# Optimization experiments

Measured on AMD Instinct MI355X. Metric: run time of the kernel, lower is better.

## Reference

```python
import jax, jax.numpy as jnp
import numpy as np

B, D_IN = 16384, 1024
N_DOM, EMB = 4, 16
H1, H2, H3 = 512, 256, 128
FH = 64
EPS = 1e-5


def setup_inputs() -> dict:
    key = jax.random.key(0)
    ks = jax.random.split(key, 32)
    s = 0.02
    def rn(k, shape):
        return jax.random.normal(k, shape, dtype=jnp.float32) * s
    inp = {
        "x": jax.random.normal(ks[0], (B, D_IN), dtype=jnp.float32),
        "domain_ids": jax.random.randint(ks[1], (B,), 0, N_DOM),
        # PartitionedNormalization params
        "pn_w": jnp.ones((N_DOM, D_IN), jnp.float32),
        "pn_b": jnp.zeros((N_DOM, D_IN), jnp.float32),
        # center net: D_IN->512->256->128
        "cW1": rn(ks[2], (D_IN, H1)), "cb1": jnp.zeros((H1,), jnp.float32),
        "cW2": rn(ks[3], (H1, H2)),  "cb2": jnp.zeros((H2,), jnp.float32),
        "cW3": rn(ks[4], (H2, H3)),  "cb3": jnp.zeros((H3,), jnp.float32),
        # domain-specific nets, stacked over domains
        "dW1": rn(ks[5], (N_DOM, D_IN, H1)), "db1": jnp.zeros((N_DOM, H1), jnp.float32),
        "dW2": rn(ks[6], (N_DOM, H1, H2)),  "db2": jnp.zeros((N_DOM, H2), jnp.float32),
        "dW3": rn(ks[7], (N_DOM, H2, H3)),  "db3": jnp.full((N_DOM, H3), 1.0, jnp.float32),  # domain_net_init_bias=1.0
        # final mlp: 128->64->1
        "fW1": rn(ks[8], (H3, FH)), "fb1": jnp.zeros((FH,), jnp.float32),
        "fW2": rn(ks[9], (FH, 1)),  "fb2": jnp.zeros((1,), jnp.float32),
        # domain embedding + auxiliary net: 16->32->1
        "dom_emb": rn(ks[10], (N_DOM, EMB)),
        "aW1": rn(ks[11], (EMB, 32)), "ab1": jnp.zeros((32,), jnp.float32),
        "aW2": rn(ks[12], (32, 1)),   "ab2": jnp.zeros((1,), jnp.float32),
    }
    return inp


def _forward(x, domain_ids, pn_w, pn_b,
             cW1, cb1, cW2, cb2, cW3, cb3,
             dW1, db1, dW2, db2, dW3, db3,
             fW1, fb1, fW2, fb2,
             dom_emb, aW1, ab1, aW2, ab2):
    # Partitioned normalization: per-sample layernorm over features,
    # domain-conditional affine (vectorized gather instead of python loop)
    mean = jnp.mean(x, axis=1, keepdims=True)
    var = jnp.mean(jnp.square(x - mean), axis=1, keepdims=True)  # unbiased=False
    norm = (x - mean) / jnp.sqrt(var + EPS)
    norm = norm * pn_w[domain_ids] + pn_b[domain_ids]  # (B, D_IN)

    # center net
    h = jax.nn.relu(norm @ cW1 + cb1)
    h = jax.nn.relu(h @ cW2 + cb2)
    h_center = h @ cW3 + cb3  # (B, H3)

    # domain-specific nets: compute all domains, then gather per-sample
    hd = jax.nn.relu(jnp.einsum('bi,dio->bdo', norm, dW1) + db1[None])   # (B,D,H1)
    hd = jax.nn.relu(jnp.einsum('bdi,dio->bdo', hd, dW2) + db2[None])    # (B,D,H2)
    hd = jnp.einsum('bdi,dio->bdo', hd, dW3) + db3[None]                 # (B,D,H3)
    h_domain = jnp.take_along_axis(hd, domain_ids[:, None, None], axis=1)[:, 0]  # (B,H3)

    h_fused = h_center * jnp.tanh(h_domain)

    main = jax.nn.relu(h_fused @ fW1 + fb1) @ fW2 + fb2  # (B,1)

    de = dom_emb[domain_ids]                              # (B,EMB)
    aux = jax.nn.relu(de @ aW1 + ab1) @ aW2 + ab2         # (B,1)

    return jax.nn.sigmoid(main + aux)


def reference(x, domain_ids, pn_w, pn_b,
              cW1, cb1, cW2, cb2, cW3, cb3,
              dW1, db1, dW2, db2, dW3, db3,
              fW1, fb1, fW2, fb2,
              dom_emb, aW1, ab1, aW2, ab2):
    return _forward(x, domain_ids, pn_w, pn_b,
                    cW1, cb1, cW2, cb2, cW3, cb3,
                    dW1, db1, dW2, db2, dW3, db3,
                    fW1, fb1, fW2, fb2,
                    dom_emb, aW1, ab1, aW2, ab2)
```

## Files before the change

kernel.cpp:

```cpp
#include <hip/hip_runtime.h>
#include <hip/hip_bf16.h>
#include <stdint.h>

#define NB   16384
#define DIN  1024
#define MPAD 16896

typedef __bf16 bf16;
typedef __bf16 v8bf __attribute__((ext_vector_type(8)));
typedef float  v4f  __attribute__((ext_vector_type(4)));
typedef unsigned char u8;

typedef __attribute__((address_space(1))) void* as1_ptr;
typedef __attribute__((address_space(3))) void* as3_ptr;

__device__ __forceinline__ void gl_lds16(const void* g, void* l) {
  __builtin_amdgcn_global_load_lds((as1_ptr)(g), (as3_ptr)(l), 16, 0, 0);
}

__device__ __forceinline__ unsigned short bfbits(float f) {
  bf16 h = (bf16)f;
  return __builtin_bit_cast(unsigned short, h);
}

__device__ __forceinline__ unsigned short pk8(float a, float b) {
  int u = __builtin_amdgcn_cvt_pk_fp8_f32(a, b, 0, false);
  return (unsigned short)(u & 0xffff);
}

__global__ __launch_bounds__(1024) void k_sort(
    const int* __restrict__ dom, int* __restrict__ pstart_g,
    int* __restrict__ perm, int* __restrict__ rowpos, float* __restrict__ aux,
    const float* __restrict__ dom_emb, const float* __restrict__ aW1,
    const float* __restrict__ ab1, const float* __restrict__ aW2,
    const float* __restrict__ ab2) {
  __shared__ int sc0[1024], sc1[1024], sc2[1024], sc3[1024];
  const int tid = threadIdx.x;
  int dv[16];
  int c0 = 0, c1 = 0, c2 = 0, c3 = 0;
#pragma unroll
  for (int it = 0; it < 16; it++) {
    int d = dom[it * 1024 + tid];
    dv[it] = d;
    c0 += (d == 0); c1 += (d == 1); c2 += (d == 2); c3 += (d == 3);
  }
  sc0[tid] = c0; sc1[tid] = c1; sc2[tid] = c2; sc3[tid] = c3;
  for (int j = tid; j < MPAD; j += 1024) perm[j] = -1;
  __syncthreads();
  for (int off = 1; off < 1024; off <<= 1) {
    int v0 = (tid >= off) ? sc0[tid - off] : 0;
    int v1 = (tid >= off) ? sc1[tid - off] : 0;
    int v2 = (tid >= off) ? sc2[tid - off] : 0;
    int v3 = (tid >= off) ? sc3[tid - off] : 0;
    __syncthreads();
    sc0[tid] += v0; sc1[tid] += v1; sc2[tid] += v2; sc3[tid] += v3;
    __syncthreads();
  }
  const int t0 = sc0[1023], t1 = sc1[1023], t2 = sc2[1023];
  const int s1 = (t0 + 127) & ~127;
  const int s2 = s1 + ((t1 + 127) & ~127);
  const int s3 = s2 + ((t2 + 127) & ~127);
  int b0 = 0 + sc0[tid] - c0;
  int b1 = s1 + sc1[tid] - c1;
  int b2 = s2 + sc2[tid] - c2;
  int b3 = s3 + sc3[tid] - c3;
#pragma unroll
  for (int it = 0; it < 16; it++) {
    int i = it * 1024 + tid;
    int d = dv[it];
    int pos = (d == 0) ? b0++ : ((d == 1) ? b1++ : ((d == 2) ? b2++ : b3++));
    perm[pos] = i;
    rowpos[i] = pos;
  }
  if (tid == 0) {
    int t3 = sc3[1023];
    pstart_g[0] = 0; pstart_g[1] = s1; pstart_g[2] = s2; pstart_g[3] = s3;
    pstart_g[4] = s3 + ((t3 + 127) & ~127);
  }
  if (tid < 4) {
    float a = ab2[0];
    for (int j = 0; j < 32; j++) {
      float s = ab1[j];
      for (int i = 0; i < 16; i++) s += dom_emb[tid * 16 + i] * aW1[i * 32 + j];
      a += fmaxf(s, 0.f) * aW2[j];
    }
    aux[tid] = a;
  }
}

__global__ __launch_bounds__(256) void k_ln(const float* __restrict__ x,
                                            const int* __restrict__ dom,
                                            const int* __restrict__ rowpos,
                                            const float* __restrict__ pn_w,
                                            const float* __restrict__ pn_b,
                                            u8* __restrict__ norm) {
  int wv = threadIdx.x >> 6, lane = threadIdx.x & 63;
  int r = blockIdx.x * 4 + wv;
  const float* xr = x + (size_t)r * DIN;
  float4 v[4];
#pragma unroll
  for (int g = 0; g < 4; g++) v[g] = *(const float4*)(xr + g * 256 + lane * 4);
  float s = 0.f;
#pragma unroll
  for (int g = 0; g < 4; g++) s += v[g].x + v[g].y + v[g].z + v[g].w;
#pragma unroll
  for (int o = 32; o; o >>= 1) s += __shfl_xor(s, o, 64);
  float mean = s * (1.f / 1024.f);
  float q = 0.f;
#pragma unroll
  for (int g = 0; g < 4; g++) {
    float a = v[g].x - mean, b = v[g].y - mean, c = v[g].z - mean, e = v[g].w - mean;
    q += a * a + b * b + c * c + e * e;
  }
#pragma unroll
  for (int o = 32; o; o >>= 1) q += __shfl_xor(q, o, 64);
  float rstd = rsqrtf(q * (1.f / 1024.f) + 1e-5f);
  int d = dom[r];
  int pos = rowpos[r];
  const float* pw = pn_w + (size_t)d * DIN;
  const float* pb = pn_b + (size_t)d * DIN;
  u8* orow = norm + (size_t)pos * DIN;
#pragma unroll
  for (int g = 0; g < 4; g++) {
    float4 w4 = *(const float4*)(pw + g * 256 + lane * 4);
    float4 b4 = *(const float4*)(pb + g * 256 + lane * 4);
    float f0 = (v[g].x - mean) * rstd * w4.x + b4.x;
    float f1 = (v[g].y - mean) * rstd * w4.y + b4.y;
    float f2 = (v[g].z - mean) * rstd * w4.z + b4.z;
    float f3 = (v[g].w - mean) * rstd * w4.w + b4.w;
    int u = __builtin_amdgcn_cvt_pk_fp8_f32(f0, f1, 0, false);
    u = __builtin_amdgcn_cvt_pk_fp8_f32(f2, f3, u, true);
    *(unsigned int*)(orow + g * 256 + lane * 4) = (unsigned int)u;
  }
}

__global__ __launch_bounds__(256) void k_wt_all(
    const float* __restrict__ cW1, const float* __restrict__ cW2,
    const float* __restrict__ cW3, const float* __restrict__ dW1,
    const float* __restrict__ dW2, const float* __restrict__ dW3,
    const float* __restrict__ fW1,
    u8* __restrict__ cW1t, u8* __restrict__ cW2t, u8* __restrict__ cW3t,
    u8* __restrict__ dW1t, u8* __restrict__ dW2t, u8* __restrict__ dW3t,
    bf16* __restrict__ fW1t) {
  __shared__ float t[64 * 65];
  int bid = blockIdx.x;
  const float* src; u8* dst; int K, N, tile; bool isf = false;
  if (bid < 640) {
    K = 1024; N = 512; int m = bid >> 7; tile = bid & 127;
    src = m == 0 ? cW1 : dW1 + (size_t)(m - 1) * 524288;
    dst = m == 0 ? cW1t : dW1t + (size_t)(m - 1) * 524288;
  } else if (bid < 800) {
    K = 512; N = 256; int m = (bid - 640) >> 5; tile = (bid - 640) & 31;
    src = m == 0 ? cW2 : dW2 + (size_t)(m - 1) * 131072;
    dst = m == 0 ? cW2t : dW2t + (size_t)(m - 1) * 131072;
  } else if (bid < 840) {
    K = 256; N = 128; int m = (bid - 800) >> 3; tile = (bid - 800) & 7;
    src = m == 0 ? cW3 : dW3 + (size_t)(m - 1) * 32768;
    dst = m == 0 ? cW3t : dW3t + (size_t)(m - 1) * 32768;
  } else {
    K = 128; N = 64; tile = bid - 840; src = fW1; dst = nullptr; isf = true;
  }
  int ntn = N >> 6;
  int k0 = (tile / ntn) << 6, n0 = (tile % ntn) << 6;
  int tid = threadIdx.x;
  int r = tid >> 2, c4 = (tid & 3) << 4;
#pragma unroll
  for (int j4 = 0; j4 < 4; j4++) {
    float4 v = *(const float4*)(src + (size_t)(k0 + r) * N + n0 + c4 + j4 * 4);
    t[r * 65 + c4 + j4 * 4 + 0] = v.x;
    t[r * 65 + c4 + j4 * 4 + 1] = v.y;
    t[r * 65 + c4 + j4 * 4 + 2] = v.z;
    t[r * 65 + c4 + j4 * 4 + 3] = v.w;
  }
  __syncthreads();
  int n = tid >> 2, kc = (tid & 3) << 4;
  if (!isf) {
#pragma unroll
    for (int j4 = 0; j4 < 4; j4++) {
      float v0 = t[(kc + j4 * 4 + 0) * 65 + n] * 16.f;
      float v1 = t[(kc + j4 * 4 + 1) * 65 + n] * 16.f;
      float v2 = t[(kc + j4 * 4 + 2) * 65 + n] * 16.f;
      float v3 = t[(kc + j4 * 4 + 3) * 65 + n] * 16.f;
      int u = __builtin_amdgcn_cvt_pk_fp8_f32(v0, v1, 0, false);
      u = __builtin_amdgcn_cvt_pk_fp8_f32(v2, v3, u, true);
      *(unsigned int*)(dst + (size_t)(n0 + n) * K + k0 + kc + j4 * 4) = (unsigned int)u;
    }
  } else {
#pragma unroll
    for (int j4 = 0; j4 < 4; j4++) {
      ushort4 o;
      o.x = bfbits(t[(kc + j4 * 4 + 0) * 65 + n]);
      o.y = bfbits(t[(kc + j4 * 4 + 1) * 65 + n]);
      o.z = bfbits(t[(kc + j4 * 4 + 2) * 65 + n]);
      o.w = bfbits(t[(kc + j4 * 4 + 3) * 65 + n]);
      *(ushort4*)(fW1t + (size_t)(n0 + n) * K + k0 + kc + j4 * 4) = o;
    }
  }
}

__global__ __launch_bounds__(256) void k_gemm(const u8* __restrict__ A, int lda,
                                              int aoffc, int aoffd,
                                              const u8* __restrict__ cWt,
                                              const u8* __restrict__ dWt,
                                              const float* __restrict__ cb,
                                              const float* __restrict__ db,
                                              u8* __restrict__ C, int Nh, int Kd,
                                              int relu, const int* __restrict__ pstart,
                                              int lognct) {
  __shared__ __align__(16) u8 Al[128 * 64];
  __shared__ __align__(16) u8 Bl[128 * 64];
  const int tid = threadIdx.x;
  const int wv = tid >> 6, lane = tid & 63;
  const int nct = 1 << lognct;
  const int T1 = nct << 7;
  int l = blockIdx.x, rt, ct;
  if (l < T1) {
    int t = l >> 3;
    ct = t & (nct - 1);
    rt = ((t >> lognct) << 3) | (l & 7);
  } else {
    int l2 = l - T1;
    rt = 128 + (l2 >> lognct);
    ct = l2 & (nct - 1);
  }
  const int row0 = rt * 128;
  int d = 0;
  if (row0 >= pstart[1]) d = 1;
  if (row0 >= pstart[2]) d = 2;
  if (row0 >= pstart[3]) d = 3;
  const int n0 = ct * 128;
  const bool isd = (n0 >= Nh);
  const u8* Wt = isd ? dWt + ((size_t)d * Nh + (n0 - Nh)) * Kd : cWt + (size_t)n0 * Kd;
  const float* bias = isd ? db + d * Nh + (n0 - Nh) : cb + n0;
  const int aoff = isd ? aoffd : aoffc;
  const u8* Ab = A + (size_t)row0 * lda + aoff;

  v4f acc[4][4];
#pragma unroll
  for (int i = 0; i < 4; i++)
#pragma unroll
    for (int j = 0; j < 4; j++) acc[i][j] = v4f{0.f, 0.f, 0.f, 0.f};

  const int wm = (wv >> 1) * 64, wn = (wv & 1) * 64;
  const int mrow = lane & 15, quad = lane >> 4;
  const int lrow = lane >> 2;
  const int lchk = lane & 3;
  const int ldc = 2 * Nh;

  for (int kt = 0; kt < Kd; kt += 64) {
#pragma unroll
    for (int p = 0; p < 2; p++) {
      int rbase = wv * 32 + p * 16;
      int r = rbase + lrow;
      int jg = lchk ^ (r & 3);
      gl_lds16(Ab + (size_t)r * lda + kt + jg * 16, &Al[rbase * 64]);
      gl_lds16(Wt + (size_t)r * Kd + kt + jg * 16, &Bl[rbase * 64]);
    }
    __syncthreads();
#pragma unroll
    for (int s = 0; s < 2; s++) {
      long af[4], bfr[4];
#pragma unroll
      for (int mi = 0; mi < 4; mi++) {
        int m = wm + mi * 16 + mrow;
        int jc = s * 2 + (quad >> 1);
        int js = jc ^ (m & 3);
        af[mi] = *(const long*)&Al[m * 64 + js * 16 + (quad & 1) * 8];
      }
#pragma unroll
      for (int ni = 0; ni < 4; ni++) {
        int n = wn + ni * 16 + mrow;
        int jc = s * 2 + (quad >> 1);
        int js = jc ^ (n & 3);
        bfr[ni] = *(const long*)&Bl[n * 64 + js * 16 + (quad & 1) * 8];
      }
#pragma unroll
      for (int mi = 0; mi < 4; mi++)
#pragma unroll
        for (int ni = 0; ni < 4; ni++)
          acc[mi][ni] =
              __builtin_amdgcn_mfma_f32_16x16x32_fp8_fp8(af[mi], bfr[ni], acc[mi][ni], 0, 0, 0);
    }
    __syncthreads();
  }

  float bv[4];
#pragma unroll
  for (int ni = 0; ni < 4; ni++) bv[ni] = bias[wn + ni * 16 + mrow];
#pragma unroll
  for (int mi = 0; mi < 4; mi++) {
    int growb = row0 + wm + mi * 16 + quad * 4;
#pragma unroll
    for (int ni = 0; ni < 4; ni++) {
      int gcol = n0 + wn + ni * 16 + mrow;
#pragma unroll
      for (int r2 = 0; r2 < 4; r2++) {
        float v = acc[mi][ni][r2] * 0.0625f + bv[ni];
        if (relu) v = fmaxf(v, 0.f);
        float g = __shfl_xor(v, 1, 64);
        if (!(mrow & 1))
          *(unsigned short*)(C + (size_t)(growb + r2) * ldc + gcol) = pk8(v, g);
      }
    }
  }
}

__global__ __launch_bounds__(256) void k_gemm3(const u8* __restrict__ A,
                                               const u8* __restrict__ cW3t,
                                               const u8* __restrict__ dW3t,
                                               const float* __restrict__ cb3,
                                               const float* __restrict__ db3,
                                               const bf16* __restrict__ fW1t,
                                               const float* __restrict__ fb1,
                                               const float* __restrict__ fW2,
                                               const float* __restrict__ fb2,
                                               const int* __restrict__ perm,
                                               const int* __restrict__ pstart,
                                               const float* __restrict__ aux,
                                               float* __restrict__ out) {
  __shared__ __align__(16) u8 Al[64 * 64];
  __shared__ __align__(16) u8 Bl[128 * 64];
  __shared__ __align__(16) bf16 fusedL[64 * 128];
  __shared__ __align__(16) bf16 fwB[64 * 128];
  const int tid = threadIdx.x, wv = tid >> 6, lane = tid & 63;
  const int row0 = blockIdx.x * 64;
  const int d = (row0 >= pstart[1]) + (row0 >= pstart[2]) + (row0 >= pstart[3]);
  const u8* Ab = A + (size_t)row0 * 512;
  const int mrow = lane & 15, quad = lane >> 4;
  const int lrow = lane >> 2, lchk = lane & 3;
  const int wm = (wv >> 1) * 32, wn = (wv & 1) * 64;

  {
    int c = lane & 15, rsub = lane >> 4;
#pragma unroll
    for (int p = 0; p < 4; p++) {
      int rbase = wv * 16 + p * 4;
      int row = rbase + rsub;
      int g = (c & 8) | ((c ^ row) & 7);
      gl_lds16(fW1t + row * 128 + g * 8, &fwB[rbase * 128]);
    }
  }

  v4f accC[2][4], accD[2][4];
#pragma unroll
  for (int i = 0; i < 2; i++)
#pragma unroll
    for (int j = 0; j < 4; j++) { accC[i][j] = v4f{0.f,0.f,0.f,0.f}; accD[i][j] = v4f{0.f,0.f,0.f,0.f}; }

#pragma unroll
  for (int ph = 0; ph < 2; ph++) {
    const u8* Wt = ph ? dW3t + (size_t)d * 32768 : cW3t;
    const int aoff = ph * 256;
    for (int kt = 0; kt < 256; kt += 64) {
      {
        int rbase = wv * 16;
        int r = rbase + lrow;
        int jg = lchk ^ (r & 3);
        gl_lds16(Ab + (size_t)r * 512 + aoff + kt + jg * 16, &Al[rbase * 64]);
      }
#pragma unroll
      for (int p = 0; p < 2; p++) {
        int rbase = wv * 32 + p * 16;
        int r = rbase + lrow;
        int jg = lchk ^ (r & 3);
        gl_lds16(Wt + (size_t)r * 256 + kt + jg * 16, &Bl[rbase * 64]);
      }
      __syncthreads();
#pragma unroll
      for (int s = 0; s < 2; s++) {
        long af[2], bfr[4];
#pragma unroll
        for (int mi = 0; mi < 2; mi++) {
          int m = wm + mi * 16 + mrow;
          int jc = s * 2 + (quad >> 1);
          int js = jc ^ (m & 3);
          af[mi] = *(const long*)&Al[m * 64 + js * 16 + (quad & 1) * 8];
        }
#pragma unroll
        for (int ni = 0; ni < 4; ni++) {
          int n = wn + ni * 16 + mrow;
          int jc = s * 2 + (quad >> 1);
          int js = jc ^ (n & 3);
          bfr[ni] = *(const long*)&Bl[n * 64 + js * 16 + (quad & 1) * 8];
        }
        if (ph == 0) {
#pragma unroll
          for (int mi = 0; mi < 2; mi++)
#pragma unroll
            for (int ni = 0; ni < 4; ni++)
              accC[mi][ni] = __builtin_amdgcn_mfma_f32_16x16x32_fp8_fp8(af[mi], bfr[ni], accC[mi][ni], 0, 0, 0);
        } else {
#pragma unroll
          for (int mi = 0; mi < 2; mi++)
#pragma unroll
            for (int ni = 0; ni < 4; ni++)
              accD[mi][ni] = __builtin_amdgcn_mfma_f32_16x16x32_fp8_fp8(af[mi], bfr[ni], accD[mi][ni], 0, 0, 0);
        }
      }
      __syncthreads();
    }
  }

#pragma unroll
  for (int mi = 0; mi < 2; mi++) {
    int rowb = wm + mi * 16 + quad * 4;
#pragma unroll
    for (int ni = 0; ni < 4; ni++) {
      int col = wn + ni * 16 + mrow;
      float cbv = cb3[col];
      float dbv = db3[d * 128 + col];
      int jc = col >> 3, coff = col & 7;
#pragma unroll
      for (int r2 = 0; r2 < 4; r2++) {
        int rr = rowb + r2;
        float f = (accC[mi][ni][r2] * 0.0625f + cbv) * tanhf(accD[mi][ni][r2] * 0.0625f + dbv);
        int cs = (jc & 8) | ((jc ^ rr) & 7);
        fusedL[rr * 128 + cs * 8 + coff] = (bf16)f;
      }
    }
  }
  __syncthreads();

  float fb1v[4], fW2v[4];
#pragma unroll
  for (int nt = 0; nt < 4; nt++) {
    int col = nt * 16 + mrow;
    fb1v[nt] = fb1[col];
    fW2v[nt] = fW2[col];
  }
  v4f hacc[4];
#pragma unroll
  for (int nt = 0; nt < 4; nt++) hacc[nt] = v4f{0.f, 0.f, 0.f, 0.f};
  const int m = wv * 16 + mrow;
#pragma unroll
  for (int s = 0; s < 4; s++) {
    int j = s * 4 + quad;
    int ca = (j & 8) | ((j ^ m) & 7);
    v8bf af = *(const v8bf*)&fusedL[m * 128 + ca * 8];
#pragma unroll
    for (int nt = 0; nt < 4; nt++) {
      int n = nt * 16 + mrow;
      int cbk = (j & 8) | ((j ^ n) & 7);
      v8bf bfr = *(const v8bf*)&fwB[n * 128 + cbk * 8];
      hacc[nt] = __builtin_amdgcn_mfma_f32_16x16x32_bf16(af, bfr, hacc[nt], 0, 0, 0);
    }
  }
  float ys[4];
#pragma unroll
  for (int r2 = 0; r2 < 4; r2++) {
    float s = 0.f;
#pragma unroll
    for (int nt = 0; nt < 4; nt++) s += fmaxf(hacc[nt][r2] + fb1v[nt], 0.f) * fW2v[nt];
    ys[r2] = s;
  }
#pragma unroll
  for (int o = 1; o < 16; o <<= 1)
#pragma unroll
    for (int r2 = 0; r2 < 4; r2++) ys[r2] += __shfl_xor(ys[r2], o, 64);
  if (mrow == 0) {
    const float addc = fb2[0] + aux[d];
#pragma unroll
    for (int r2 = 0; r2 < 4; r2++) {
      int prow = row0 + wv * 16 + quad * 4 + r2;
      int orig = perm[prow];
      if (orig >= 0) out[orig] = 1.f / (1.f + expf(-(ys[r2] + addc)));
    }
  }
}

extern "C" void kernel_launch(void* const* d_in, const int* in_sizes, int n_in,
                              void* d_out, int out_size, void* d_ws, size_t ws_size,
                              hipStream_t stream) {
  (void)in_sizes; (void)n_in; (void)out_size; (void)ws_size;
  const float* x      = (const float*)d_in[0];
  const int*   dom    = (const int*)d_in[1];
  const float* pn_w   = (const float*)d_in[2];
  const float* pn_b   = (const float*)d_in[3];
  const float* cW1    = (const float*)d_in[4];
  const float* cb1    = (const float*)d_in[5];
  const float* cW2    = (const float*)d_in[6];
  const float* cb2    = (const float*)d_in[7];
  const float* cW3    = (const float*)d_in[8];
  const float* cb3    = (const float*)d_in[9];
  const float* dW1    = (const float*)d_in[10];
  const float* db1    = (const float*)d_in[11];
  const float* dW2    = (const float*)d_in[12];
  const float* db2    = (const float*)d_in[13];
  const float* dW3    = (const float*)d_in[14];
  const float* db3    = (const float*)d_in[15];
  const float* fW1    = (const float*)d_in[16];
  const float* fb1    = (const float*)d_in[17];
  const float* fW2    = (const float*)d_in[18];
  const float* fb2    = (const float*)d_in[19];
  const float* demb   = (const float*)d_in[20];
  const float* aW1    = (const float*)d_in[21];
  const float* ab1    = (const float*)d_in[22];
  const float* aW2    = (const float*)d_in[23];
  const float* ab2    = (const float*)d_in[24];
  float* out = (float*)d_out;

  char* w = (char*)d_ws;
  int*   pstart = (int*)(w + 32);
  float* aux    = (float*)(w + 64);
  int*   perm   = (int*)(w + 256);
  int*   rowpos = (int*)(w + 67840);
  u8*    bufA   = (u8*)(w + 133376);
  u8*    bufB   = (u8*)(w + 17434880);
  u8*    cW1t   = (u8*)(w + 34736384);
  u8*    cW2t   = (u8*)(w + 35260672);
  u8*    cW3t   = (u8*)(w + 35391744);
  u8*    dW1t   = (u8*)(w + 35424512);
  u8*    dW2t   = (u8*)(w + 37521664);
  u8*    dW3t   = (u8*)(w + 38045952);
  bf16*  fW1t   = (bf16*)(w + 38177024);

  k_sort<<<1, 1024, 0, stream>>>(dom, pstart, perm, rowpos, aux,
                                 demb, aW1, ab1, aW2, ab2);
  k_ln<<<4096, 256, 0, stream>>>(x, dom, rowpos, pn_w, pn_b, bufA);
  k_wt_all<<<842, 256, 0, stream>>>(cW1, cW2, cW3, dW1, dW2, dW3, fW1,
                                    cW1t, cW2t, cW3t, dW1t, dW2t, dW3t, fW1t);

  k_gemm<<<1056, 256, 0, stream>>>(bufA, 1024, 0, 0, cW1t, dW1t, cb1, db1,
                                   bufB, 512, 1024, 1, pstart, 3);
  k_gemm<<<528, 256, 0, stream>>>(bufB, 1024, 0, 512, cW2t, dW2t, cb2, db2,
                                  bufA, 256, 512, 1, pstart, 2);
  k_gemm3<<<264, 256, 0, stream>>>(bufA, cW3t, dW3t, cb3, db3, fW1t,
                                   fb1, fW2, fb2, perm, pstart, aux, out);
}
```

Before: 254.4 us.

## Parallelize domain sort and retile GEMMs to 64-row, 128-wide K tiles

```diff
diff --git a/kernel.cpp b/kernel.cpp
--- a/kernel.cpp
+++ b/kernel.cpp
@@ -9,6 +9,7 @@
 typedef __bf16 bf16;
 typedef __bf16 v8bf __attribute__((ext_vector_type(8)));
 typedef float  v4f  __attribute__((ext_vector_type(4)));
+typedef long   v2l  __attribute__((ext_vector_type(2)));
 typedef unsigned char u8;
 
 typedef __attribute__((address_space(1))) void* as1_ptr;
@@ -28,54 +29,38 @@
   return (unsigned short)(u & 0xffff);
 }
 
-__global__ __launch_bounds__(1024) void k_sort(
-    const int* __restrict__ dom, int* __restrict__ pstart_g,
-    int* __restrict__ perm, int* __restrict__ rowpos, float* __restrict__ aux,
+__global__ __launch_bounds__(1024) void k_histscan_aux(
+    const int* __restrict__ dom, int* __restrict__ pstart, int* __restrict__ cnt2,
+    int* __restrict__ perm, float* __restrict__ aux,
     const float* __restrict__ dom_emb, const float* __restrict__ aW1,
     const float* __restrict__ ab1, const float* __restrict__ aW2,
     const float* __restrict__ ab2) {
-  __shared__ int sc0[1024], sc1[1024], sc2[1024], sc3[1024];
-  const int tid = threadIdx.x;
-  int dv[16];
+  __shared__ int hist[4];
+  int tid = threadIdx.x, lane = tid & 63;
+  if (tid < 4) hist[tid] = 0;
+  if (tid >= 8 && tid < 12) cnt2[tid - 8] = 0;
+  for (int j = tid; j < MPAD; j += 1024) perm[j] = -1;
+  __syncthreads();
   int c0 = 0, c1 = 0, c2 = 0, c3 = 0;
 #pragma unroll
   for (int it = 0; it < 16; it++) {
     int d = dom[it * 1024 + tid];
-    dv[it] = d;
     c0 += (d == 0); c1 += (d == 1); c2 += (d == 2); c3 += (d == 3);
   }
-  sc0[tid] = c0; sc1[tid] = c1; sc2[tid] = c2; sc3[tid] = c3;
-  for (int j = tid; j < MPAD; j += 1024) perm[j] = -1;
+#pragma unroll
+  for (int o = 32; o; o >>= 1) {
+    c0 += __shfl_xor(c0, o, 64); c1 += __shfl_xor(c1, o, 64);
+    c2 += __shfl_xor(c2, o, 64); c3 += __shfl_xor(c3, o, 64);
+  }
+  if (lane == 0) {
+    atomicAdd(&hist[0], c0); atomicAdd(&hist[1], c1);
+    atomicAdd(&hist[2], c2); atomicAdd(&hist[3], c3);
+  }
   __syncthreads();
-  for (int off = 1; off < 1024; off <<= 1) {
-    int v0 = (tid >= off) ? sc0[tid - off] : 0;
-    int v1 = (tid >= off) ? sc1[tid - off] : 0;
-    int v2 = (tid >= off) ? sc2[tid - off] : 0;
-    int v3 = (tid >= off) ? sc3[tid - off] : 0;
-    __syncthreads();
-    sc0[tid] += v0; sc1[tid] += v1; sc2[tid] += v2; sc3[tid] += v3;
-    __syncthreads();
-  }
-  const int t0 = sc0[1023], t1 = sc1[1023], t2 = sc2[1023];
-  const int s1 = (t0 + 127) & ~127;
-  const int s2 = s1 + ((t1 + 127) & ~127);
-  const int s3 = s2 + ((t2 + 127) & ~127);
-  int b0 = 0 + sc0[tid] - c0;
-  int b1 = s1 + sc1[tid] - c1;
-  int b2 = s2 + sc2[tid] - c2;
-  int b3 = s3 + sc3[tid] - c3;
-#pragma unroll
-  for (int it = 0; it < 16; it++) {
-    int i = it * 1024 + tid;
-    int d = dv[it];
-    int pos = (d == 0) ? b0++ : ((d == 1) ? b1++ : ((d == 2) ? b2++ : b3++));
-    perm[pos] = i;
-    rowpos[i] = pos;
-  }
   if (tid == 0) {
-    int t3 = sc3[1023];
-    pstart_g[0] = 0; pstart_g[1] = s1; pstart_g[2] = s2; pstart_g[3] = s3;
-    pstart_g[4] = s3 + ((t3 + 127) & ~127);
+    int p = 0;
+    for (int d = 0; d < 4; d++) { pstart[d] = p; p += (hist[d] + 127) & ~127; }
+    pstart[4] = p;
   }
   if (tid < 4) {
     float a = ab2[0];
@@ -85,6 +70,28 @@
       a += fmaxf(s, 0.f) * aW2[j];
     }
     aux[tid] = a;
+  }
+}
+
+__global__ void k_assign(const int* __restrict__ dom, const int* __restrict__ pstart,
+                         int* __restrict__ cnt2, int* __restrict__ perm,
+                         int* __restrict__ rowpos) {
+  int i = blockIdx.x * 256 + threadIdx.x;
+  int lane = threadIdx.x & 63;
+  int d = dom[i];
+  unsigned long long ltmask = (1ull << lane) - 1ull;
+#pragma unroll
+  for (int dd = 0; dd < 4; dd++) {
+    unsigned long long m = __ballot(d == dd);
+    int c = __popcll(m);
+    int base = 0;
+    if (lane == 0 && c) base = atomicAdd(&cnt2[dd], c);
+    base = __shfl(base, 0, 64);
+    if (d == dd) {
+      int pos = pstart[dd] + base + __popcll(m & ltmask);
+      perm[pos] = i;
+      rowpos[i] = pos;
+    }
   }
 }
 
@@ -207,27 +214,17 @@
                                               u8* __restrict__ C, int Nh, int Kd,
                                               int relu, const int* __restrict__ pstart,
                                               int lognct) {
-  __shared__ __align__(16) u8 Al[128 * 64];
-  __shared__ __align__(16) u8 Bl[128 * 64];
+  __shared__ __align__(16) u8 Al[64 * 128];
+  __shared__ __align__(16) u8 Bl[128 * 128];
   const int tid = threadIdx.x;
   const int wv = tid >> 6, lane = tid & 63;
   const int nct = 1 << lognct;
-  const int T1 = nct << 7;
-  int l = blockIdx.x, rt, ct;
-  if (l < T1) {
-    int t = l >> 3;
-    ct = t & (nct - 1);
-    rt = ((t >> lognct) << 3) | (l & 7);
-  } else {
-    int l2 = l - T1;
-    rt = 128 + (l2 >> lognct);
-    ct = l2 & (nct - 1);
-  }
-  const int row0 = rt * 128;
-  int d = 0;
-  if (row0 >= pstart[1]) d = 1;
-  if (row0 >= pstart[2]) d = 2;
-  if (row0 >= pstart[3]) d = 3;
+  int l = blockIdx.x;
+  int t = l >> 3;
+  int ct = t & (nct - 1);
+  int rt = ((t >> lognct) << 3) | (l & 7);
+  const int row0 = rt * 64;
+  const int d = (row0 >= pstart[1]) + (row0 >= pstart[2]) + (row0 >= pstart[3]);
   const int n0 = ct * 128;
   const bool isd = (n0 >= Nh);
   const u8* Wt = isd ? dWt + ((size_t)d * Nh + (n0 - Nh)) * Kd : cWt + (size_t)n0 * Kd;
@@ -235,51 +232,61 @@
   const int aoff = isd ? aoffd : aoffc;
   const u8* Ab = A + (size_t)row0 * lda + aoff;
 
-  v4f acc[4][4];
-#pragma unroll
-  for (int i = 0; i < 4; i++)
+  v4f acc[2][4];
+#pragma unroll
+  for (int i = 0; i < 2; i++)
 #pragma unroll
     for (int j = 0; j < 4; j++) acc[i][j] = v4f{0.f, 0.f, 0.f, 0.f};
 
-  const int wm = (wv >> 1) * 64, wn = (wv & 1) * 64;
+  const int wm = (wv >> 1) * 32, wn = (wv & 1) * 64;
   const int mrow = lane & 15, quad = lane >> 4;
-  const int lrow = lane >> 2;
-  const int lchk = lane & 3;
+  const int lrow = lane >> 3;
+  const int lchk = lane & 7;
   const int ldc = 2 * Nh;
 
-  for (int kt = 0; kt < Kd; kt += 64) {
+  for (int kt = 0; kt < Kd; kt += 128) {
 #pragma unroll
     for (int p = 0; p < 2; p++) {
-      int rbase = wv * 32 + p * 16;
+      int rbase = wv * 16 + p * 8;
       int r = rbase + lrow;
-      int jg = lchk ^ (r & 3);
-      gl_lds16(Ab + (size_t)r * lda + kt + jg * 16, &Al[rbase * 64]);
-      gl_lds16(Wt + (size_t)r * Kd + kt + jg * 16, &Bl[rbase * 64]);
+      int jg = lchk ^ (r & 7);
+      gl_lds16(Ab + (size_t)r * lda + kt + jg * 16, &Al[rbase * 128]);
+    }
+#pragma unroll
+    for (int p = 0; p < 4; p++) {
+      int rbase = wv * 32 + p * 8;
+      int r = rbase + lrow;
+      int jg = lchk ^ (r & 7);
+      gl_lds16(Wt + (size_t)r * Kd + kt + jg * 16, &Bl[rbase * 128]);
     }
     __syncthreads();
 #pragma unroll
-    for (int s = 0; s < 2; s++) {
-      long af[4], bfr[4];
-#pragma unroll
-      for (int mi = 0; mi < 4; mi++) {
+    for (int sp = 0; sp < 2; sp++) {
+      v2l af[2], bfr[4];
+#pragma unroll
+      for (int mi = 0; mi < 2; mi++) {
         int m = wm + mi * 16 + mrow;
-        int jc = s * 2 + (quad >> 1);
-        int js = jc ^ (m & 3);
-        af[mi] = *(const long*)&Al[m * 64 + js * 16 + (quad & 1) * 8];
+        int c = (sp * 4 + quad) ^ (m & 7);
+        af[mi] = *(const v2l*)&Al[m * 128 + c * 16];
       }
 #pragma unroll
       for (int ni = 0; ni < 4; ni++) {
         int n = wn + ni * 16 + mrow;
-        int jc = s * 2 + (quad >> 1);
-        int js = jc ^ (n & 3);
-        bfr[ni] = *(const long*)&Bl[n * 64 + js * 16 + (quad & 1) * 8];
-      }
-#pragma unroll
-      for (int mi = 0; mi < 4; mi++)
+        int c = (sp * 4 + quad) ^ (n & 7);
+        bfr[ni] = *(const v2l*)&Bl[n * 128 + c * 16];
+      }
+#pragma unroll
+      for (int mi = 0; mi < 2; mi++)
 #pragma unroll
         for (int ni = 0; ni < 4; ni++)
           acc[mi][ni] =
-              __builtin_amdgcn_mfma_f32_16x16x32_fp8_fp8(af[mi], bfr[ni], acc[mi][ni], 0, 0, 0);
+              __builtin_amdgcn_mfma_f32_16x16x32_fp8_fp8(af[mi].x, bfr[ni].x, acc[mi][ni], 0, 0, 0);
+#pragma unroll
+      for (int mi = 0; mi < 2; mi++)
+#pragma unroll
+        for (int ni = 0; ni < 4; ni++)
+          acc[mi][ni] =
+              __builtin_amdgcn_mfma_f32_16x16x32_fp8_fp8(af[mi].y, bfr[ni].y, acc[mi][ni], 0, 0, 0);
     }
     __syncthreads();
   }
@@ -288,7 +295,7 @@
 #pragma unroll
   for (int ni = 0; ni < 4; ni++) bv[ni] = bias[wn + ni * 16 + mrow];
 #pragma unroll
-  for (int mi = 0; mi < 4; mi++) {
+  for (int mi = 0; mi < 2; mi++) {
     int growb = row0 + wm + mi * 16 + quad * 4;
 #pragma unroll
     for (int ni = 0; ni < 4; ni++) {
@@ -318,8 +325,8 @@
                                                const int* __restrict__ pstart,
                                                const float* __restrict__ aux,
                                                float* __restrict__ out) {
-  __shared__ __align__(16) u8 Al[64 * 64];
-  __shared__ __align__(16) u8 Bl[128 * 64];
+  __shared__ __align__(16) u8 Al[64 * 128];
+  __shared__ __align__(16) u8 Bl[128 * 128];
   __shared__ __align__(16) bf16 fusedL[64 * 128];
   __shared__ __align__(16) bf16 fwB[64 * 128];
   const int tid = threadIdx.x, wv = tid >> 6, lane = tid & 63;
@@ -327,7 +334,7 @@
   const int d = (row0 >= pstart[1]) + (row0 >= pstart[2]) + (row0 >= pstart[3]);
   const u8* Ab = A + (size_t)row0 * 512;
   const int mrow = lane & 15, quad = lane >> 4;
-  const int lrow = lane >> 2, lchk = lane & 3;
+  const int lrow = lane >> 3, lchk = lane & 7;
   const int wm = (wv >> 1) * 32, wn = (wv & 1) * 64;
 
   {
@@ -351,50 +358,53 @@
   for (int ph = 0; ph < 2; ph++) {
     const u8* Wt = ph ? dW3t + (size_t)d * 32768 : cW3t;
     const int aoff = ph * 256;
-    for (int kt = 0; kt < 256; kt += 64) {
-      {
-        int rbase = wv * 16;
+    for (int kt = 0; kt < 256; kt += 128) {
+#pragma unroll
+      for (int p = 0; p < 2; p++) {
+        int rbase = wv * 16 + p * 8;
         int r = rbase + lrow;
-        int jg = lchk ^ (r & 3);
-        gl_lds16(Ab + (size_t)r * 512 + aoff + kt + jg * 16, &Al[rbase * 64]);
-      }
-#pragma unroll
-      for (int p = 0; p < 2; p++) {
-        int rbase = wv * 32 + p * 16;
+        int jg = lchk ^ (r & 7);
+        gl_lds16(Ab + (size_t)r * 512 + aoff + kt + jg * 16, &Al[rbase * 128]);
+      }
+#pragma unroll
+      for (int p = 0; p < 4; p++) {
+        int rbase = wv * 32 + p * 8;
         int r = rbase + lrow;
-        int jg = lchk ^ (r & 3);
-        gl_lds16(Wt + (size_t)r * 256 + kt + jg * 16, &Bl[rbase * 64]);
+        int jg = lchk ^ (r & 7);
+        gl_lds16(Wt + (size_t)r * 256 + kt + jg * 16, &Bl[rbase * 128]);
       }
       __syncthreads();
 #pragma unroll
-      for (int s = 0; s < 2; s++) {
-        long af[2], bfr[4];
+      for (int sp = 0; sp < 2; sp++) {
+        v2l af[2], bfr[4];
 #pragma unroll
         for (int mi = 0; mi < 2; mi++) {
           int m = wm + mi * 16 + mrow;
-          int jc = s * 2 + (quad >> 1);
-          int js = jc ^ (m & 3);
-          af[mi] = *(const long*)&Al[m * 64 + js * 16 + (quad & 1) * 8];
+          int c = (sp * 4 + quad) ^ (m & 7);
+          af[mi] = *(const v2l*)&Al[m * 128 + c * 16];
         }
 #pragma unroll
         for (int ni = 0; ni < 4; ni++) {
           int n = wn + ni * 16 + mrow;
-          int jc = s * 2 + (quad >> 1);
-          int js = jc ^ (n & 3);
-          bfr[ni] = *(const long*)&Bl[n * 64 + js * 16 + (quad & 1) * 8];
+          int c = (sp * 4 + quad) ^ (n & 7);
+          bfr[ni] = *(const v2l*)&Bl[n * 128 + c * 16];
         }
         if (ph == 0) {
 #pragma unroll
           for (int mi = 0; mi < 2; mi++)
 #pragma unroll
-            for (int ni = 0; ni < 4; ni++)
-              accC[mi][ni] = __builtin_amdgcn_mfma_f32_16x16x32_fp8_fp8(af[mi], bfr[ni], accC[mi][ni], 0, 0, 0);
+            for (int ni = 0; ni < 4; ni++) {
+              accC[mi][ni] = __builtin_amdgcn_mfma_f32_16x16x32_fp8_fp8(af[mi].x, bfr[ni].x, accC[mi][ni], 0, 0, 0);
+              accC[mi][ni] = __builtin_amdgcn_mfma_f32_16x16x32_fp8_fp8(af[mi].y, bfr[ni].y, accC[mi][ni], 0, 0, 0);
+            }
         } else {
 #pragma unroll
           for (int mi = 0; mi < 2; mi++)
 #pragma unroll
-            for (int ni = 0; ni < 4; ni++)
-              accD[mi][ni] = __builtin_amdgcn_mfma_f32_16x16x32_fp8_fp8(af[mi], bfr[ni], accD[mi][ni], 0, 0, 0);
+            for (int ni = 0; ni < 4; ni++) {
+              accD[mi][ni] = __builtin_amdgcn_mfma_f32_16x16x32_fp8_fp8(af[mi].x, bfr[ni].x, accD[mi][ni], 0, 0, 0);
+              accD[mi][ni] = __builtin_amdgcn_mfma_f32_16x16x32_fp8_fp8(af[mi].y, bfr[ni].y, accD[mi][ni], 0, 0, 0);
+            }
         }
       }
       __syncthreads();
@@ -500,6 +510,7 @@
   float* out = (float*)d_out;
 
   char* w = (char*)d_ws;
+  int*   cnt2   = (int*)(w + 0);
   int*   pstart = (int*)(w + 32);
   float* aux    = (float*)(w + 64);
   int*   perm   = (int*)(w + 256);
@@ -514,16 +525,17 @@
   u8*    dW3t   = (u8*)(w + 38045952);
   bf16*  fW1t   = (bf16*)(w + 38177024);
 
-  k_sort<<<1, 1024, 0, stream>>>(dom, pstart, perm, rowpos, aux,
-                                 demb, aW1, ab1, aW2, ab2);
+  k_histscan_aux<<<1, 1024, 0, stream>>>(dom, pstart, cnt2, perm, aux,
+                                         demb, aW1, ab1, aW2, ab2);
+  k_assign<<<64, 256, 0, stream>>>(dom, pstart, cnt2, perm, rowpos);
   k_ln<<<4096, 256, 0, stream>>>(x, dom, rowpos, pn_w, pn_b, bufA);
   k_wt_all<<<842, 256, 0, stream>>>(cW1, cW2, cW3, dW1, dW2, dW3, fW1,
                                     cW1t, cW2t, cW3t, dW1t, dW2t, dW3t, fW1t);
 
-  k_gemm<<<1056, 256, 0, stream>>>(bufA, 1024, 0, 0, cW1t, dW1t, cb1, db1,
+  k_gemm<<<2112, 256, 0, stream>>>(bufA, 1024, 0, 0, cW1t, dW1t, cb1, db1,
                                    bufB, 512, 1024, 1, pstart, 3);
-  k_gemm<<<528, 256, 0, stream>>>(bufB, 1024, 0, 512, cW2t, dW2t, cb2, db2,
-                                  bufA, 256, 512, 1, pstart, 2);
+  k_gemm<<<1056, 256, 0, stream>>>(bufB, 1024, 0, 512, cW2t, dW2t, cb2, db2,
+                                   bufA, 256, 512, 1, pstart, 2);
   k_gemm3<<<264, 256, 0, stream>>>(bufA, cW3t, dW3t, cb3, db3, fW1t,
                                    fb1, fW2, fb2, perm, pstart, aux, out);
 }
```

Result: faster. 235.1 us (-7.6%).
